# Optimization experiments

Hardware: AMD Instinct MI355X
Metric: run time of the kernel (lower is better)

The kernel has to match this reference:

```python
import jax, jax.numpy as jnp
import numpy as np

B = 16        # decode batch (one query token per sequence)
H = 32        # query heads
HKV = 8       # kv heads (GQA)
D = 128       # head dim
BLOCK = 256   # kv-cache block size (from module: self.block_size = 256)
MAXBLK = 16   # blocks per sequence
MAXCTX = MAXBLK * BLOCK   # 4096
NBLK = 256    # total physical blocks
NSLOTS = NBLK * BLOCK     # 65536 slots
SCALE = 1.0 / float(np.sqrt(D))
EPS = 1e-8


def setup_inputs() -> dict:
    key = jax.random.key(0)
    ks = jax.random.split(key, 10)
    q = jax.random.normal(ks[0], (B, H, D), jnp.float32)
    k = jax.random.normal(ks[1], (B, HKV, D), jnp.float32)
    v = jax.random.normal(ks[2], (B, HKV, D), jnp.float32)
    # int8 quantized KV caches, layout [HKV, NSLOTS, D] per triton kernel strides
    k_cache = jax.random.randint(ks[3], (HKV, NSLOTS, D), -127, 128).astype(jnp.int8)
    v_cache = jax.random.randint(ks[4], (HKV, NSLOTS, D), -127, 128).astype(jnp.int8)
    # per-(head, slot) dequant scales, positive
    k_scale_cache = jax.random.uniform(ks[5], (HKV, NSLOTS), jnp.float32, 1e-4, 0.03)
    v_scale_cache = jax.random.uniform(ks[6], (HKV, NSLOTS), jnp.float32, 1e-4, 0.03)
    slot_mapping = jax.random.randint(ks[7], (B,), 0, NSLOTS)
    block_table = jax.random.randint(ks[8], (B, MAXBLK), 0, NBLK)
    context_lens = jax.random.randint(ks[9], (B,), 1, MAXCTX + 1)
    return dict(q=q, k=k, v=v, k_cache=k_cache, v_cache=v_cache,
                k_scale_cache=k_scale_cache, v_scale_cache=v_scale_cache,
                slot_mapping=slot_mapping, block_table=block_table,
                context_lens=context_lens)


def _quantize(x):
    # per-(token, head) abs-max int8 quantization, matching _store_quantkv_kernel
    s = jnp.maximum(jnp.max(jnp.abs(x), axis=-1) / 127.0, EPS)
    xi = jnp.clip(jnp.round(x / s[..., None]), -127.0, 127.0).astype(jnp.int8)
    return xi, s


def reference(q, k, v, k_cache, v_cache, k_scale_cache, v_scale_cache,
              slot_mapping, block_table, context_lens):
    G = H // HKV
    # --- gather + dequantize paged KV cache (decode_attn_quantkv_direct) ---
    pos = jnp.arange(MAXCTX)                               # [S]
    slots = block_table[:, pos // BLOCK] * BLOCK + (pos % BLOCK)  # [B, S]
    K = jnp.take(k_cache, slots, axis=1).astype(jnp.float32) \
        * jnp.take(k_scale_cache, slots, axis=1)[..., None]       # [HKV, B, S, D]
    V = jnp.take(v_cache, slots, axis=1).astype(jnp.float32) \
        * jnp.take(v_scale_cache, slots, axis=1)[..., None]       # [HKV, B, S, D]
    # --- attention: cached context tokens + current (unquantized) token ---
    qr = q.reshape(B, HKV, G, D)
    lc = jnp.einsum('bhgd,hbsd->bhgs', qr, K) * SCALE             # [B, HKV, G, S]
    valid = pos[None, :] < context_lens[:, None]                  # [B, S]
    lc = jnp.where(valid[:, None, None, :], lc, -jnp.inf)
    lcur = jnp.einsum('bhgd,bhd->bhg', qr, k) * SCALE             # current token
    logits = jnp.concatenate([lc, lcur[..., None]], axis=-1)      # [B, HKV, G, S+1]
    p = jax.nn.softmax(logits, axis=-1)
    o = jnp.einsum('bhgs,hbsd->bhgd', p[..., :MAXCTX], V) \
        + p[..., MAXCTX, None] * v[:, :, None, :]
    o = o.reshape(B, H, D)
    # --- fused quantized KV-cache store (store_quantkv) ---
    kq8, ks = _quantize(k)   # [B, HKV, D], [B, HKV]
    vq8, vs = _quantize(v)
    kc = k_cache.at[:, slot_mapping, :].set(jnp.transpose(kq8, (1, 0, 2)))
    vc = v_cache.at[:, slot_mapping, :].set(jnp.transpose(vq8, (1, 0, 2)))
    ksc = k_scale_cache.at[:, slot_mapping].set(ks.T)
    vsc = v_scale_cache.at[:, slot_mapping].set(vs.T)
    return (o, kc, vc, ksc, vsc)
```

## Files before the change

### kernel.cpp

```cpp
#include <hip/hip_runtime.h>
#include <hip/hip_fp16.h>
#include <stdint.h>

#define BB      16
#define HH      32
#define HKVN    8
#define GG      4
#define DD      128
#define BLK     256
#define MAXBLKN 16
#define MAXCTXN 4096
#define NSLOTSN 65536
#define ATT_SCALE 0.08838834764831845f
#define QEPS    1e-8f

#define NSPLIT  16
#define CHUNK   256

#define O_OFF   0
#define KC_OFF  65536
#define VC_OFF  (65536 + 67108864)
#define KSC_OFF (65536 + 2*67108864)
#define VSC_OFF (65536 + 2*67108864 + 524288)

#define WS_M    0
#define WS_L    8192
#define WS_O    16384

#define NREG    (HKVN * 256)
#define NOVF    (256 * HKVN)

typedef float f32x4 __attribute__((ext_vector_type(4)));

__global__ __launch_bounds__(256) void fused_kernel(
    const float* __restrict__ q,
    const int* __restrict__ k_cache, const int* __restrict__ v_cache,
    const float* __restrict__ k_scale, const float* __restrict__ v_scale,
    const int* __restrict__ block_table, const int* __restrict__ context_lens,
    float* __restrict__ ws, float* __restrict__ out) {
  const int bid = blockIdx.x;
  const int tid = threadIdx.x;

  __shared__ __align__(16) float q_s[GG][DD];
  __shared__ __half p_s[GG][CHUNK];
  __shared__ float racc[8][32][17];
  __shared__ float red[GG][4];
  __shared__ int minpair;
  __shared__ int ovf_p;

  int h, b, s;
  bool do_partial = false;

  if (bid < NREG) {
    h = bid >> 8;
    const int p = bid & 255;
    if (tid == 0) minpair = 0x7fffffff;
    __syncthreads();
    if (block_table[tid] == p && (tid & 15) * CHUNK < context_lens[tid >> 4])
      atomicMin(&minpair, tid);

    const int reg = h * NSLOTSN + p * BLK;
    {
      const int4* srcK = (const int4*)k_cache + (size_t)reg * 32;
      const int4* srcV = (const int4*)v_cache + (size_t)reg * 32;
      f32x4* dstK = (f32x4*)(out + KC_OFF) + (size_t)reg * 32;
      f32x4* dstV = (f32x4*)(out + VC_OFF) + (size_t)reg * 32;
#pragma unroll 4
      for (int i = 0; i < 32; ++i) {
        int4 w = srcK[i * 256 + tid];
        f32x4 f;
        f.x = (float)w.x; f.y = (float)w.y; f.z = (float)w.z; f.w = (float)w.w;
        __builtin_nontemporal_store(f, dstK + i * 256 + tid);
      }
#pragma unroll 4
      for (int i = 0; i < 32; ++i) {
        int4 w = srcV[i * 256 + tid];
        f32x4 f;
        f.x = (float)w.x; f.y = (float)w.y; f.z = (float)w.z; f.w = (float)w.w;
        __builtin_nontemporal_store(f, dstV + i * 256 + tid);
      }
      if (tid < 64) {
        float4 w0 = ((const float4*)k_scale)[reg / 4 + tid];
        f32x4 w; w.x = w0.x; w.y = w0.y; w.z = w0.z; w.w = w0.w;
        __builtin_nontemporal_store(w, (f32x4*)(out + KSC_OFF) + reg / 4 + tid);
      } else if (tid < 128) {
        float4 w0 = ((const float4*)v_scale)[reg / 4 + (tid - 64)];
        f32x4 w; w.x = w0.x; w.y = w0.y; w.z = w0.z; w.w = w0.w;
        __builtin_nontemporal_store(w, (f32x4*)(out + VSC_OFF) + reg / 4 + (tid - 64));
      }
    }
    __syncthreads();
    if (minpair == 0x7fffffff) return;
    b = minpair >> 4;
    s = minpair & 15;
    do_partial = true;
  } else {
    const int idx = bid - NREG;
    const int pi = idx >> 3;
    h = idx & 7;
    b = pi >> 4;
    s = pi & 15;
    if (s * CHUNK >= context_lens[b]) return;
    if (tid == 0) {
      minpair = 0x7fffffff;
      ovf_p = block_table[pi];
    }
    __syncthreads();
    const int p = ovf_p;
    if (block_table[tid] == p && (tid & 15) * CHUNK < context_lens[tid >> 4])
      atomicMin(&minpair, tid);
    __syncthreads();
    if (minpair == pi) return;
    do_partial = true;
  }

  if (!do_partial) return;

  const int bh = b * HKVN + h;
  const int ctx = context_lens[b];
  const int n = min(CHUNK, ctx - s * CHUNK);
  const int base = block_table[b * MAXBLKN + s] * BLK;
  const int lane = tid & 63;
  const int wid = tid >> 6;
  const int qlane = lane & 3;
  const int quad = lane >> 2;

  for (int i = tid; i < GG * DD; i += 256)
    q_s[i >> 7][i & 127] = q[(b * HH + h * GG + (i >> 7)) * DD + (i & 127)];
  __syncthreads();

  float lmax[GG] = {-1e30f, -1e30f, -1e30f, -1e30f};
#pragma unroll
  for (int it = 0; it < 4; ++it) {
    const int tok = it * 64 + wid * 16 + quad;
    const bool active = tok < n;
    const int slot = base + tok;
    float dot[GG] = {0.f, 0.f, 0.f, 0.f};
    if (active) {
      const int4* kr = (const int4*)(k_cache + (size_t)(h * NSLOTSN + slot) * DD);
#pragma unroll
      for (int kk = 0; kk < 8; ++kk) {
        int4 w = kr[qlane + 4 * kk];
        float k0 = (float)w.x, k1 = (float)w.y, k2 = (float)w.z, k3 = (float)w.w;
        const int c = (qlane + 4 * kk) * 4;
#pragma unroll
        for (int g = 0; g < GG; ++g) {
          float4 qv = *(const float4*)&q_s[g][c];
          dot[g] += qv.x * k0 + qv.y * k1 + qv.z * k2 + qv.w * k3;
        }
      }
    }
#pragma unroll
    for (int g = 0; g < GG; ++g) {
      dot[g] += __shfl_xor(dot[g], 1);
      dot[g] += __shfl_xor(dot[g], 2);
    }
    if (active && qlane == 0) {
      float mult = k_scale[h * NSLOTSN + slot] * ATT_SCALE;
#pragma unroll
      for (int g = 0; g < GG; ++g) {
        float l = dot[g] * mult;
        p_s[g][tok] = __float2half(l);
        lmax[g] = fmaxf(lmax[g], l);
      }
    }
  }
#pragma unroll
  for (int g = 0; g < GG; ++g)
    for (int off = 32; off; off >>= 1)
      lmax[g] = fmaxf(lmax[g], __shfl_xor(lmax[g], off));
  if (lane == 0)
#pragma unroll
    for (int g = 0; g < GG; ++g) red[g][wid] = lmax[g];
  __syncthreads();
  float m[GG];
#pragma unroll
  for (int g = 0; g < GG; ++g)
    m[g] = fmaxf(fmaxf(red[g][0], red[g][1]), fmaxf(red[g][2], red[g][3]));

  float lsum[GG] = {0.f, 0.f, 0.f, 0.f};
  if (tid < n) {
#pragma unroll
    for (int g = 0; g < GG; ++g) {
      float e = __expf(__half2float(p_s[g][tid]) - m[g]);
      p_s[g][tid] = __float2half(e);
      lsum[g] += e;
    }
  }
#pragma unroll
  for (int g = 0; g < GG; ++g)
    for (int off = 32; off; off >>= 1) lsum[g] += __shfl_xor(lsum[g], off);
  __syncthreads();
  if (lane == 0)
#pragma unroll
    for (int g = 0; g < GG; ++g) red[g][wid] = lsum[g];
  __syncthreads();
  float l[GG];
#pragma unroll
  for (int g = 0; g < GG; ++g)
    l[g] = red[g][0] + red[g][1] + red[g][2] + red[g][3];

  const int vlane = tid & 31;
  const int grp = tid >> 5;
  float acc[GG][4] = {};
  const int vhb = h * NSLOTSN;
#pragma unroll 4
  for (int i = grp; i < n; i += 8) {
    int slot = base + i;
    float vs = v_scale[vhb + slot];
    int4 w = *(const int4*)(v_cache + (size_t)(vhb + slot) * DD + 4 * vlane);
    float v0 = (float)w.x * vs, v1 = (float)w.y * vs,
          v2 = (float)w.z * vs, v3 = (float)w.w * vs;
#pragma unroll
    for (int g = 0; g < GG; ++g) {
      float pw = __half2float(p_s[g][i]);
      acc[g][0] += pw * v0; acc[g][1] += pw * v1;
      acc[g][2] += pw * v2; acc[g][3] += pw * v3;
    }
  }
#pragma unroll
  for (int g = 0; g < GG; ++g)
#pragma unroll
    for (int j = 0; j < 4; ++j)
      racc[grp][vlane][g * 4 + j] = acc[g][j];
  __syncthreads();
  for (int oidx = tid; oidx < 512; oidx += 256) {
    int gj = oidx & 15;
    int vl = oidx >> 4;
    float sacc = 0.f;
#pragma unroll
    for (int rr = 0; rr < 8; ++rr) sacc += racc[rr][vl][gj];
    int g = gj >> 2, j = gj & 3;
    ws[WS_O + (((bh * GG + g) * NSPLIT + s) * DD) + (vl * 4 + j)] = sacc;
  }
  if (tid == 0) {
#pragma unroll
    for (int g = 0; g < GG; ++g) {
      ws[WS_M + (bh * GG + g) * NSPLIT + s] = m[g];
      ws[WS_L + (bh * GG + g) * NSPLIT + s] = l[g];
    }
  }
}

__global__ __launch_bounds__(128) void finish_kernel(
    const float* __restrict__ q, const float* __restrict__ kin,
    const float* __restrict__ vin, const int* __restrict__ slot_mapping,
    const int* __restrict__ context_lens, float* __restrict__ out,
    const float* __restrict__ ws) {
  const int d = threadIdx.x;
  __shared__ float red[DD];
  __shared__ float lcur_s[GG];

  if (blockIdx.x < 128) {
    const int bh = blockIdx.x;
    const int h = bh & 7;
    const int b = bh >> 3;
    const int ctx = context_lens[b];
    const int nsp = (ctx + CHUNK - 1) / CHUNK;
    if (d < GG) {
      float dc = 0.f;
      const float* qp = q + (b * HH + h * GG + d) * DD;
      const float* kp = kin + (b * HKVN + h) * DD;
      for (int j = 0; j < DD; ++j) dc += qp[j] * kp[j];
      lcur_s[d] = dc * ATT_SCALE;
    }
    __syncthreads();
    float vcur = vin[(b * HKVN + h) * DD + d];
#pragma unroll
    for (int g = 0; g < GG; ++g) {
      float lc = lcur_s[g];
      float M = lc;
      for (int s = 0; s < nsp; ++s)
        M = fmaxf(M, ws[WS_M + (bh * GG + g) * NSPLIT + s]);
      float denom = __expf(lc - M);
      float o = denom * vcur;
      for (int s = 0; s < nsp; ++s) {
        float w = __expf(ws[WS_M + (bh * GG + g) * NSPLIT + s] - M);
        denom += ws[WS_L + (bh * GG + g) * NSPLIT + s] * w;
        o += ws[WS_O + ((bh * GG + g) * NSPLIT + s) * DD + d] * w;
      }
      out[O_OFF + (b * HH + h * GG + g) * DD + d] = o / denom;
    }
  } else {
    const int sid = blockIdx.x - 128;
    const int b = sid >> 3;
    const int h = sid & 7;
    const int slot = slot_mapping[b];
    for (int b2 = b + 1; b2 < BB; ++b2)
      if (slot_mapping[b2] == slot) return;

    float xk = kin[(b * HKVN + h) * DD + d];
    red[d] = fabsf(xk);
    __syncthreads();
    for (int off = 64; off; off >>= 1) {
      if (d < off) red[d] = fmaxf(red[d], red[d + off]);
      __syncthreads();
    }
    float sk = fmaxf(red[0] / 127.0f, QEPS);
    __syncthreads();
    float qk = fminf(fmaxf(rintf(xk / sk), -127.0f), 127.0f);
    out[KC_OFF + (h * NSLOTSN + slot) * DD + d] = qk;
    if (d == 0) out[KSC_OFF + h * NSLOTSN + slot] = sk;

    float xv = vin[(b * HKVN + h) * DD + d];
    red[d] = fabsf(xv);
    __syncthreads();
    for (int off = 64; off; off >>= 1) {
      if (d < off) red[d] = fmaxf(red[d], red[d + off]);
      __syncthreads();
    }
    float sv = fmaxf(red[0] / 127.0f, QEPS);
    float qv = fminf(fmaxf(rintf(xv / sv), -127.0f), 127.0f);
    out[VC_OFF + (h * NSLOTSN + slot) * DD + d] = qv;
    if (d == 0) out[VSC_OFF + h * NSLOTSN + slot] = sv;
  }
}

extern "C" void kernel_launch(void* const* d_in, const int* in_sizes, int n_in,
                              void* d_out, int out_size, void* d_ws, size_t ws_size,
                              hipStream_t stream) {
  const float* q = (const float*)d_in[0];
  const float* k = (const float*)d_in[1];
  const float* v = (const float*)d_in[2];
  const int* k_cache = (const int*)d_in[3];
  const int* v_cache = (const int*)d_in[4];
  const float* k_scale = (const float*)d_in[5];
  const float* v_scale = (const float*)d_in[6];
  const int* slot_mapping = (const int*)d_in[7];
  const int* block_table = (const int*)d_in[8];
  const int* context_lens = (const int*)d_in[9];
  float* out = (float*)d_out;
  float* ws = (float*)d_ws;

  hipLaunchKernelGGL(fused_kernel, dim3(NREG + NOVF), dim3(256), 0, stream,
                     q, k_cache, v_cache, k_scale, v_scale,
                     block_table, context_lens, ws, out);
  hipLaunchKernelGGL(finish_kernel, dim3(256), dim3(128), 0, stream,
                     q, k, v, slot_mapping, context_lens, out, ws);
}
```

Baseline: 266.8 us.

## Fuse attention compute into the cache-copy pass to reuse loaded KV registers

Blocks that copy a physical KV region now compute the attention partial directly from the int8 values they already load for the copy. Before, they re-read K/V from global memory after the copy. Scales are staged into shared memory during the scale copy. The dot products now use a 32-lane shuffle reduction per token. This removes a second read of K/V for the primary owner of each block, at the cost of extra shuffles and a different thread mapping in the QK pass.

```diff
diff --git a/kernel.cpp b/kernel.cpp
--- a/kernel.cpp
+++ b/kernel.cpp
@@ -45,61 +45,196 @@
   __shared__ __half p_s[GG][CHUNK];
   __shared__ float racc[8][32][17];
   __shared__ float red[GG][4];
+  __shared__ __align__(16) float ks_s[CHUNK];
+  __shared__ __align__(16) float vs_s[CHUNK];
   __shared__ int minpair;
   __shared__ int ovf_p;
 
-  int h, b, s;
-  bool do_partial = false;
+  const int lane = tid & 63;
+  const int wid = tid >> 6;
 
   if (bid < NREG) {
-    h = bid >> 8;
+    const int h = bid >> 8;
     const int p = bid & 255;
     if (tid == 0) minpair = 0x7fffffff;
     __syncthreads();
     if (block_table[tid] == p && (tid & 15) * CHUNK < context_lens[tid >> 4])
       atomicMin(&minpair, tid);
-
+    __syncthreads();
+    const int mp = minpair;
+    const bool hp = (mp != 0x7fffffff);
     const int reg = h * NSLOTSN + p * BLK;
-    {
-      const int4* srcK = (const int4*)k_cache + (size_t)reg * 32;
-      const int4* srcV = (const int4*)v_cache + (size_t)reg * 32;
-      f32x4* dstK = (f32x4*)(out + KC_OFF) + (size_t)reg * 32;
-      f32x4* dstV = (f32x4*)(out + VC_OFF) + (size_t)reg * 32;
+
+    if (tid < 64) {
+      float4 w0 = ((const float4*)k_scale)[reg / 4 + tid];
+      ((float4*)ks_s)[tid] = w0;
+      f32x4 w; w.x = w0.x; w.y = w0.y; w.z = w0.z; w.w = w0.w;
+      __builtin_nontemporal_store(w, (f32x4*)(out + KSC_OFF) + reg / 4 + tid);
+    } else if (tid < 128) {
+      float4 w0 = ((const float4*)v_scale)[reg / 4 + (tid - 64)];
+      ((float4*)vs_s)[tid - 64] = w0;
+      f32x4 w; w.x = w0.x; w.y = w0.y; w.z = w0.z; w.w = w0.w;
+      __builtin_nontemporal_store(w, (f32x4*)(out + VSC_OFF) + reg / 4 + (tid - 64));
+    }
+
+    int b = 0, s = 0, n = 0;
+    if (hp) {
+      b = mp >> 4;
+      s = mp & 15;
+      n = min(CHUNK, context_lens[b] - s * CHUNK);
+      for (int i = tid; i < GG * DD; i += 256)
+        q_s[i >> 7][i & 127] = q[(b * HH + h * GG + (i >> 7)) * DD + (i & 127)];
+    }
+    __syncthreads();
+
+    const int g5 = tid >> 5;
+    const int j5 = tid & 31;
+    const int d0 = 4 * j5;
+
+    const int4* srcK = (const int4*)k_cache + (size_t)reg * 32;
+    const int4* srcV = (const int4*)v_cache + (size_t)reg * 32;
+    f32x4* dstK = (f32x4*)(out + KC_OFF) + (size_t)reg * 32;
+    f32x4* dstV = (f32x4*)(out + VC_OFF) + (size_t)reg * 32;
+
+    if (!hp) {
 #pragma unroll 4
       for (int i = 0; i < 32; ++i) {
-        int4 w = srcK[i * 256 + tid];
+        const int u = i * 256 + tid;
+        int4 w = srcK[u];
         f32x4 f;
         f.x = (float)w.x; f.y = (float)w.y; f.z = (float)w.z; f.w = (float)w.w;
-        __builtin_nontemporal_store(f, dstK + i * 256 + tid);
+        __builtin_nontemporal_store(f, dstK + u);
       }
 #pragma unroll 4
       for (int i = 0; i < 32; ++i) {
-        int4 w = srcV[i * 256 + tid];
+        const int u = i * 256 + tid;
+        int4 w = srcV[u];
         f32x4 f;
         f.x = (float)w.x; f.y = (float)w.y; f.z = (float)w.z; f.w = (float)w.w;
-        __builtin_nontemporal_store(f, dstV + i * 256 + tid);
-      }
-      if (tid < 64) {
-        float4 w0 = ((const float4*)k_scale)[reg / 4 + tid];
-        f32x4 w; w.x = w0.x; w.y = w0.y; w.z = w0.z; w.w = w0.w;
-        __builtin_nontemporal_store(w, (f32x4*)(out + KSC_OFF) + reg / 4 + tid);
-      } else if (tid < 128) {
-        float4 w0 = ((const float4*)v_scale)[reg / 4 + (tid - 64)];
-        f32x4 w; w.x = w0.x; w.y = w0.y; w.z = w0.z; w.w = w0.w;
-        __builtin_nontemporal_store(w, (f32x4*)(out + VSC_OFF) + reg / 4 + (tid - 64));
-      }
-    }
-    __syncthreads();
-    if (minpair == 0x7fffffff) return;
-    b = minpair >> 4;
-    s = minpair & 15;
-    do_partial = true;
-  } else {
+        __builtin_nontemporal_store(f, dstV + u);
+      }
+      return;
+    }
+
+    float qv[GG][4];
+#pragma unroll
+    for (int g = 0; g < GG; ++g)
+#pragma unroll
+      for (int j = 0; j < 4; ++j) qv[g][j] = q_s[g][d0 + j];
+    float lmax[GG] = {-1e30f, -1e30f, -1e30f, -1e30f};
+#pragma unroll 4
+    for (int i = 0; i < 32; ++i) {
+      const int u = i * 256 + tid;
+      int4 w = srcK[u];
+      f32x4 f;
+      f.x = (float)w.x; f.y = (float)w.y; f.z = (float)w.z; f.w = (float)w.w;
+      __builtin_nontemporal_store(f, dstK + u);
+      const int tok = i * 8 + g5;
+      float dot[GG];
+#pragma unroll
+      for (int g = 0; g < GG; ++g)
+        dot[g] = qv[g][0] * f.x + qv[g][1] * f.y + qv[g][2] * f.z + qv[g][3] * f.w;
+#pragma unroll
+      for (int off = 1; off <= 16; off <<= 1)
+#pragma unroll
+        for (int g = 0; g < GG; ++g) dot[g] += __shfl_xor(dot[g], off);
+      if (tok < n) {
+        const float mult = ks_s[tok] * ATT_SCALE;
+#pragma unroll
+        for (int g = 0; g < GG; ++g) {
+          float lg = dot[g] * mult;
+          lmax[g] = fmaxf(lmax[g], lg);
+          if (j5 == 0) p_s[g][tok] = __float2half(lg);
+        }
+      }
+    }
+#pragma unroll
+    for (int g = 0; g < GG; ++g)
+      for (int off = 32; off; off >>= 1)
+        lmax[g] = fmaxf(lmax[g], __shfl_xor(lmax[g], off));
+    if (lane == 0)
+#pragma unroll
+      for (int g = 0; g < GG; ++g) red[g][wid] = lmax[g];
+    __syncthreads();
+    float m[GG];
+#pragma unroll
+    for (int g = 0; g < GG; ++g)
+      m[g] = fmaxf(fmaxf(red[g][0], red[g][1]), fmaxf(red[g][2], red[g][3]));
+
+    float lsum[GG] = {0.f, 0.f, 0.f, 0.f};
+    if (tid < n) {
+#pragma unroll
+      for (int g = 0; g < GG; ++g) {
+        float e = __expf(__half2float(p_s[g][tid]) - m[g]);
+        p_s[g][tid] = __float2half(e);
+        lsum[g] += e;
+      }
+    }
+#pragma unroll
+    for (int g = 0; g < GG; ++g)
+      for (int off = 32; off; off >>= 1) lsum[g] += __shfl_xor(lsum[g], off);
+    __syncthreads();
+    if (lane == 0)
+#pragma unroll
+      for (int g = 0; g < GG; ++g) red[g][wid] = lsum[g];
+    __syncthreads();
+    float l[GG];
+#pragma unroll
+    for (int g = 0; g < GG; ++g)
+      l[g] = red[g][0] + red[g][1] + red[g][2] + red[g][3];
+
+    float acc[GG][4] = {};
+#pragma unroll 4
+    for (int i = 0; i < 32; ++i) {
+      const int u = i * 256 + tid;
+      int4 w = srcV[u];
+      f32x4 f;
+      f.x = (float)w.x; f.y = (float)w.y; f.z = (float)w.z; f.w = (float)w.w;
+      __builtin_nontemporal_store(f, dstV + u);
+      const int tok = i * 8 + g5;
+      if (tok < n) {
+        const float vs = vs_s[tok];
+        const float f0 = f.x * vs, f1 = f.y * vs, f2 = f.z * vs, f3 = f.w * vs;
+#pragma unroll
+        for (int g = 0; g < GG; ++g) {
+          const float pw = __half2float(p_s[g][tok]);
+          acc[g][0] += pw * f0; acc[g][1] += pw * f1;
+          acc[g][2] += pw * f2; acc[g][3] += pw * f3;
+        }
+      }
+    }
+#pragma unroll
+    for (int g = 0; g < GG; ++g)
+#pragma unroll
+      for (int j = 0; j < 4; ++j)
+        racc[g5][j5][g * 4 + j] = acc[g][j];
+    __syncthreads();
+    const int bh = b * HKVN + h;
+    for (int oidx = tid; oidx < 512; oidx += 256) {
+      int gj = oidx & 15;
+      int vl = oidx >> 4;
+      float sacc = 0.f;
+#pragma unroll
+      for (int rr = 0; rr < 8; ++rr) sacc += racc[rr][vl][gj];
+      int g = gj >> 2, j = gj & 3;
+      ws[WS_O + (((bh * GG + g) * NSPLIT + s) * DD) + (vl * 4 + j)] = sacc;
+    }
+    if (tid == 0) {
+#pragma unroll
+      for (int g = 0; g < GG; ++g) {
+        ws[WS_M + (bh * GG + g) * NSPLIT + s] = m[g];
+        ws[WS_L + (bh * GG + g) * NSPLIT + s] = l[g];
+      }
+    }
+    return;
+  }
+
+  {
     const int idx = bid - NREG;
     const int pi = idx >> 3;
-    h = idx & 7;
-    b = pi >> 4;
-    s = pi & 15;
+    const int h = idx & 7;
+    const int b = pi >> 4;
+    const int s = pi & 15;
     if (s * CHUNK >= context_lens[b]) return;
     if (tid == 0) {
       minpair = 0x7fffffff;
@@ -111,133 +246,128 @@
       atomicMin(&minpair, tid);
     __syncthreads();
     if (minpair == pi) return;
-    do_partial = true;
-  }
-
-  if (!do_partial) return;
-
-  const int bh = b * HKVN + h;
-  const int ctx = context_lens[b];
-  const int n = min(CHUNK, ctx - s * CHUNK);
-  const int base = block_table[b * MAXBLKN + s] * BLK;
-  const int lane = tid & 63;
-  const int wid = tid >> 6;
-  const int qlane = lane & 3;
-  const int quad = lane >> 2;
-
-  for (int i = tid; i < GG * DD; i += 256)
-    q_s[i >> 7][i & 127] = q[(b * HH + h * GG + (i >> 7)) * DD + (i & 127)];
-  __syncthreads();
-
-  float lmax[GG] = {-1e30f, -1e30f, -1e30f, -1e30f};
-#pragma unroll
-  for (int it = 0; it < 4; ++it) {
-    const int tok = it * 64 + wid * 16 + quad;
-    const bool active = tok < n;
-    const int slot = base + tok;
-    float dot[GG] = {0.f, 0.f, 0.f, 0.f};
-    if (active) {
-      const int4* kr = (const int4*)(k_cache + (size_t)(h * NSLOTSN + slot) * DD);
-#pragma unroll
-      for (int kk = 0; kk < 8; ++kk) {
-        int4 w = kr[qlane + 4 * kk];
-        float k0 = (float)w.x, k1 = (float)w.y, k2 = (float)w.z, k3 = (float)w.w;
-        const int c = (qlane + 4 * kk) * 4;
+
+    const int bh = b * HKVN + h;
+    const int ctx = context_lens[b];
+    const int n = min(CHUNK, ctx - s * CHUNK);
+    const int base = p * BLK;
+    const int qlane = lane & 3;
+    const int quad = lane >> 2;
+
+    for (int i = tid; i < GG * DD; i += 256)
+      q_s[i >> 7][i & 127] = q[(b * HH + h * GG + (i >> 7)) * DD + (i & 127)];
+    __syncthreads();
+
+    float lmax[GG] = {-1e30f, -1e30f, -1e30f, -1e30f};
+#pragma unroll
+    for (int it = 0; it < 4; ++it) {
+      const int tok = it * 64 + wid * 16 + quad;
+      const bool active = tok < n;
+      const int slot = base + tok;
+      float dot[GG] = {0.f, 0.f, 0.f, 0.f};
+      if (active) {
+        const int4* kr = (const int4*)(k_cache + (size_t)(h * NSLOTSN + slot) * DD);
+#pragma unroll
+        for (int kk = 0; kk < 8; ++kk) {
+          int4 w = kr[qlane + 4 * kk];
+          float k0 = (float)w.x, k1 = (float)w.y, k2 = (float)w.z, k3 = (float)w.w;
+          const int c = (qlane + 4 * kk) * 4;
+#pragma unroll
+          for (int g = 0; g < GG; ++g) {
+            float4 qv = *(const float4*)&q_s[g][c];
+            dot[g] += qv.x * k0 + qv.y * k1 + qv.z * k2 + qv.w * k3;
+          }
+        }
+      }
+#pragma unroll
+      for (int g = 0; g < GG; ++g) {
+        dot[g] += __shfl_xor(dot[g], 1);
+        dot[g] += __shfl_xor(dot[g], 2);
+      }
+      if (active && qlane == 0) {
+        float mult = k_scale[h * NSLOTSN + slot] * ATT_SCALE;
 #pragma unroll
         for (int g = 0; g < GG; ++g) {
-          float4 qv = *(const float4*)&q_s[g][c];
-          dot[g] += qv.x * k0 + qv.y * k1 + qv.z * k2 + qv.w * k3;
+          float lg = dot[g] * mult;
+          p_s[g][tok] = __float2half(lg);
+          lmax[g] = fmaxf(lmax[g], lg);
         }
       }
     }
 #pragma unroll
-    for (int g = 0; g < GG; ++g) {
-      dot[g] += __shfl_xor(dot[g], 1);
-      dot[g] += __shfl_xor(dot[g], 2);
-    }
-    if (active && qlane == 0) {
-      float mult = k_scale[h * NSLOTSN + slot] * ATT_SCALE;
-#pragma unroll
-      for (int g = 0; g < GG; ++g) {
-        float l = dot[g] * mult;
-        p_s[g][tok] = __float2half(l);
-        lmax[g] = fmaxf(lmax[g], l);
-      }
-    }
-  }
-#pragma unroll
-  for (int g = 0; g < GG; ++g)
-    for (int off = 32; off; off >>= 1)
-      lmax[g] = fmaxf(lmax[g], __shfl_xor(lmax[g], off));
-  if (lane == 0)
-#pragma unroll
-    for (int g = 0; g < GG; ++g) red[g][wid] = lmax[g];
-  __syncthreads();
-  float m[GG];
-#pragma unroll
-  for (int g = 0; g < GG; ++g)
-    m[g] = fmaxf(fmaxf(red[g][0], red[g][1]), fmaxf(red[g][2], red[g][3]));
-
-  float lsum[GG] = {0.f, 0.f, 0.f, 0.f};
-  if (tid < n) {
-#pragma unroll
-    for (int g = 0; g < GG; ++g) {
-      float e = __expf(__half2float(p_s[g][tid]) - m[g]);
-      p_s[g][tid] = __float2half(e);
-      lsum[g] += e;
-    }
-  }
-#pragma unroll
-  for (int g = 0; g < GG; ++g)
-    for (int off = 32; off; off >>= 1) lsum[g] += __shfl_xor(lsum[g], off);
-  __syncthreads();
-  if (lane == 0)
-#pragma unroll
-    for (int g = 0; g < GG; ++g) red[g][wid] = lsum[g];
-  __syncthreads();
-  float l[GG];
-#pragma unroll
-  for (int g = 0; g < GG; ++g)
-    l[g] = red[g][0] + red[g][1] + red[g][2] + red[g][3];
-
-  const int vlane = tid & 31;
-  const int grp = tid >> 5;
-  float acc[GG][4] = {};
-  const int vhb = h * NSLOTSN;
+    for (int g = 0; g < GG; ++g)
+      for (int off = 32; off; off >>= 1)
+        lmax[g] = fmaxf(lmax[g], __shfl_xor(lmax[g], off));
+    if (lane == 0)
+#pragma unroll
+      for (int g = 0; g < GG; ++g) red[g][wid] = lmax[g];
+    __syncthreads();
+    float m[GG];
+#pragma unroll
+    for (int g = 0; g < GG; ++g)
+      m[g] = fmaxf(fmaxf(red[g][0], red[g][1]), fmaxf(red[g][2], red[g][3]));
+
+    float lsum[GG] = {0.f, 0.f, 0.f, 0.f};
+    if (tid < n) {
+#pragma unroll
+      for (int g = 0; g < GG; ++g) {
+        float e = __expf(__half2float(p_s[g][tid]) - m[g]);
+        p_s[g][tid] = __float2half(e);
+        lsum[g] += e;
+      }
+    }
+#pragma unroll
+    for (int g = 0; g < GG; ++g)
+      for (int off = 32; off; off >>= 1) lsum[g] += __shfl_xor(lsum[g], off);
+    __syncthreads();
+    if (lane == 0)
+#pragma unroll
+      for (int g = 0; g < GG; ++g) red[g][wid] = lsum[g];
+    __syncthreads();
+    float l[GG];
+#pragma unroll
+    for (int g = 0; g < GG; ++g)
+      l[g] = red[g][0] + red[g][1] + red[g][2] + red[g][3];
+
+    const int vlane = tid & 31;
+    const int grp = tid >> 5;
+    float acc[GG][4] = {};
+    const int vhb = h * NSLOTSN;
 #pragma unroll 4
-  for (int i = grp; i < n; i += 8) {
-    int slot = base + i;
-    float vs = v_scale[vhb + slot];
-    int4 w = *(const int4*)(v_cache + (size_t)(vhb + slot) * DD + 4 * vlane);
-    float v0 = (float)w.x * vs, v1 = (float)w.y * vs,
-          v2 = (float)w.z * vs, v3 = (float)w.w * vs;
-#pragma unroll
-    for (int g = 0; g < GG; ++g) {
-      float pw = __half2float(p_s[g][i]);
-      acc[g][0] += pw * v0; acc[g][1] += pw * v1;
-      acc[g][2] += pw * v2; acc[g][3] += pw * v3;
-    }
-  }
-#pragma unroll
-  for (int g = 0; g < GG; ++g)
-#pragma unroll
-    for (int j = 0; j < 4; ++j)
-      racc[grp][vlane][g * 4 + j] = acc[g][j];
-  __syncthreads();
-  for (int oidx = tid; oidx < 512; oidx += 256) {
-    int gj = oidx & 15;
-    int vl = oidx >> 4;
-    float sacc = 0.f;
-#pragma unroll
-    for (int rr = 0; rr < 8; ++rr) sacc += racc[rr][vl][gj];
-    int g = gj >> 2, j = gj & 3;
-    ws[WS_O + (((bh * GG + g) * NSPLIT + s) * DD) + (vl * 4 + j)] = sacc;
-  }
-  if (tid == 0) {
-#pragma unroll
-    for (int g = 0; g < GG; ++g) {
-      ws[WS_M + (bh * GG + g) * NSPLIT + s] = m[g];
-      ws[WS_L + (bh * GG + g) * NSPLIT + s] = l[g];
+    for (int i = grp; i < n; i += 8) {
+      int slot = base + i;
+      float vs = v_scale[vhb + slot];
+      int4 w = *(const int4*)(v_cache + (size_t)(vhb + slot) * DD + 4 * vlane);
+      float v0 = (float)w.x * vs, v1 = (float)w.y * vs,
+            v2 = (float)w.z * vs, v3 = (float)w.w * vs;
+#pragma unroll
+      for (int g = 0; g < GG; ++g) {
+        float pw = __half2float(p_s[g][i]);
+        acc[g][0] += pw * v0; acc[g][1] += pw * v1;
+        acc[g][2] += pw * v2; acc[g][3] += pw * v3;
+      }
+    }
+#pragma unroll
+    for (int g = 0; g < GG; ++g)
+#pragma unroll
+      for (int j = 0; j < 4; ++j)
+        racc[grp][vlane][g * 4 + j] = acc[g][j];
+    __syncthreads();
+    for (int oidx = tid; oidx < 512; oidx += 256) {
+      int gj = oidx & 15;
+      int vl = oidx >> 4;
+      float sacc = 0.f;
+#pragma unroll
+      for (int rr = 0; rr < 8; ++rr) sacc += racc[rr][vl][gj];
+      int g = gj >> 2, j = gj & 3;
+      ws[WS_O + (((bh * GG + g) * NSPLIT + s) * DD) + (vl * 4 + j)] = sacc;
+    }
+    if (tid == 0) {
+#pragma unroll
+      for (int g = 0; g < GG; ++g) {
+        ws[WS_M + (bh * GG + g) * NSPLIT + s] = m[g];
+        ws[WS_L + (bh * GG + g) * NSPLIT + s] = l[g];
+      }
     }
   }
 }
```

Measured after the change: 260.9 us. 1.02x faster.
